# Optimization experiments

Hardware: AMD Instinct MI355X
Metric: run time of the kernel (lower is better)

Reference implementation:

```python
import jax, jax.numpy as jnp
import numpy as np

H = 1024  # n_hidden
T = 8192  # sequence length


def setup_inputs() -> dict:
    key = jax.random.key(0)
    ks = jax.random.split(key, 11)
    s = 1.0 / np.sqrt(H)  # torch LSTMCell/Linear default init scale
    u = lambda k, shape: jax.random.uniform(k, shape, jnp.float32, -s, s)
    return {
        "sequence": jax.random.normal(ks[0], (1, T), jnp.float32),
        # lstm1: input size 1 -> hidden H
        "w_ih1": u(ks[1], (4 * H, 1)),
        "w_hh1": u(ks[2], (4 * H, H)),
        "b_ih1": u(ks[3], (4 * H,)),
        "b_hh1": u(ks[4], (4 * H,)),
        # lstm2: hidden H -> hidden H
        "w_ih2": u(ks[5], (4 * H, H)),
        "w_hh2": u(ks[6], (4 * H, H)),
        "b_ih2": u(ks[7], (4 * H,)),
        "b_hh2": u(ks[8], (4 * H,)),
        # final linear: H -> 1
        "w_lin": u(ks[9], (1, H)),
        "b_lin": u(ks[10], (1,)),
    }


def _lstm_cell(x, h, c, w_ih, w_hh, b_ih, b_hh):
    # x: [1, in], h/c: [1, H]. PyTorch LSTMCell gate order: i, f, g, o
    gates = x @ w_ih.T + h @ w_hh.T + (b_ih + b_hh)  # [1, 4H]
    i, f, g, o = jnp.split(gates, 4, axis=-1)
    i = jax.nn.sigmoid(i)
    f = jax.nn.sigmoid(f)
    g = jnp.tanh(g)
    o = jax.nn.sigmoid(o)
    c_new = f * c + i * g
    h_new = o * jnp.tanh(c_new)
    return h_new, c_new


def reference(sequence, w_ih1, w_hh1, b_ih1, b_hh1,
              w_ih2, w_hh2, b_ih2, b_hh2, w_lin, b_lin):
    n = sequence.shape[0]  # 1
    z = jnp.zeros((n, w_hh1.shape[1]), jnp.float32)
    init = (z, z, z, z)  # h1, c1, h2, c2
    xs = sequence.T[:, :, None]  # [T, 1, 1] timesteps

    def step(carry, x_t):
        h1, c1, h2, c2 = carry
        h1, c1 = _lstm_cell(x_t, h1, c1, w_ih1, w_hh1, b_ih1, b_hh1)
        h2, c2 = _lstm_cell(h1, h2, c2, w_ih2, w_hh2, b_ih2, b_hh2)
        out = h2 @ w_lin.T + b_lin  # [1, 1]
        return (h1, c1, h2, c2), out

    _, outputs = jax.lax.scan(step, init, xs)
    return outputs  # [T, 1, 1] — stacked version of the original list of [1,1] outputs
```

## Files before the change

kernel.cpp:

```cpp
#include <hip/hip_runtime.h>

#define HID   1024
#define SEQT  8192
#define NBLK  256
#define TPB   512

#define WS_BYTES 32768

typedef float v16f __attribute__((ext_vector_type(16)));
typedef unsigned long long u64;

__device__ __forceinline__ float sig_(float x) { return 1.0f / (1.0f + expf(-x)); }

__device__ __forceinline__ u64 ldp(const u64* p) {
    return __hip_atomic_load(p, __ATOMIC_RELAXED, __HIP_MEMORY_SCOPE_AGENT);
}
__device__ __forceinline__ void stp(u64* p, u64 v) {
    __hip_atomic_store(p, v, __ATOMIC_RELAXED, __HIP_MEMORY_SCOPE_AGENT);
}

extern "C" __global__ void __launch_bounds__(TPB, 2)
lstm_hyb(const float* __restrict__ seq,
         const float* __restrict__ w_ih1, const float* __restrict__ w_hh1,
         const float* __restrict__ b_ih1, const float* __restrict__ b_hh1,
         const float* __restrict__ w_ih2, const float* __restrict__ w_hh2,
         const float* __restrict__ b_ih2, const float* __restrict__ b_hh2,
         const float* __restrict__ w_lin, const float* __restrict__ b_lin,
         float* __restrict__ out, u64* ws)
{
    __shared__ float h1s[HID];
    __shared__ float h2s[HID];
    __shared__ float seqs[SEQT];

    const int  lane = threadIdx.x & 63;
    const int  widx = threadIdx.x >> 6;
    const bool isL1 = (widx < 4);
    const int  r    = blockIdx.x * 4 + (widx & 3);

    u64* h1t = ws;
    u64* h2t = ws + 2048;

    for (int i = threadIdx.x; i < SEQT; i += TPB) seqs[i] = seq[i];

    const float* bA  = isL1 ? w_hh1 : w_ih2;
    const float* bB  = isL1 ? w_hh1 : w_hh2;
    const float* bbi = isL1 ? b_ih1 : b_ih2;
    const float* bbh = isL1 ? b_hh1 : b_hh2;
    const float  zmask = isL1 ? 0.f : 1.f;
    const float  xsel  = isL1 ? 1.f : 0.f;

    v16f A0, A1, A2, A3, B0, B1, B2, B3;
    {
        const size_t ro = (size_t)r * HID + lane;
        const float *a0 = bA + ro, *a1 = bA + (size_t)HID * HID + ro,
                    *a2 = bA + 2 * (size_t)HID * HID + ro, *a3 = bA + 3 * (size_t)HID * HID + ro;
        const float *b0 = bB + ro, *b1 = bB + (size_t)HID * HID + ro,
                    *b2 = bB + 2 * (size_t)HID * HID + ro, *b3 = bB + 3 * (size_t)HID * HID + ro;
#pragma unroll
        for (int k = 0; k < 16; ++k) {
            A0[k] = a0[64 * k]; A1[k] = a1[64 * k]; A2[k] = a2[64 * k]; A3[k] = a3[64 * k];
            B0[k] = b0[64 * k]; B1[k] = b1[64 * k]; B2[k] = b2[64 * k]; B3[k] = b3[64 * k];
        }
    }
    const float wx0 = w_ih1[0 * HID + r], wx1 = w_ih1[1 * HID + r],
                wx2 = w_ih1[2 * HID + r], wx3 = w_ih1[3 * HID + r];
    const float bb0 = bbi[0 * HID + r] + bbh[0 * HID + r];
    const float bb1 = bbi[1 * HID + r] + bbh[1 * HID + r];
    const float bb2 = bbi[2 * HID + r] + bbh[2 * HID + r];
    const float bb3 = bbi[3 * HID + r] + bbh[3 * HID + r];

    const bool carrier = (blockIdx.x == 0 && widx == 7);
    v16f WL; float blin = 0.f;
#pragma unroll
    for (int k = 0; k < 16; ++k) WL[k] = 0.f;
    if (carrier) {
#pragma unroll
        for (int k = 0; k < 16; ++k) WL[k] = w_lin[lane + 64 * k];
        blin = b_lin[0];
    }

    u64* pub = isL1 ? h1t : h2t;
    float c = 0.f;

    for (int t = 0; t <= SEQT + 1; ++t) {
        if (widx == 0 && t <= SEQT) {
            const u64* p = h1t + ((t + 1) & 1) * HID + lane;
            int guard = 0;
            for (;;) {
                int mn = 0x7fffffff;
#pragma unroll
                for (int k = 0; k < 16; ++k) {
                    u64 q = ldp(p + 64 * k);
                    h1s[lane + 64 * k] = __uint_as_float((unsigned)q);
                    mn = min(mn, (int)(q >> 32));
                }
                if (__all(mn >= t)) break;
                if (++guard > (1 << 14)) break;
            }
        }
        if (widx == 4) {
            const u64* p = h2t + (t & 1) * HID + lane;
            const int thr = t - 1;
            int guard = 0;
            for (;;) {
                int mn = 0x7fffffff;
#pragma unroll
                for (int k = 0; k < 16; ++k) {
                    u64 q = ldp(p + 64 * k);
                    h2s[lane + 64 * k] = __uint_as_float((unsigned)q);
                    mn = min(mn, (int)(q >> 32));
                }
                if (__all(mn >= thr)) break;
                if (++guard > (1 << 14)) break;
            }
        }
        __syncthreads();

        const bool act = isL1 ? (t < SEQT) : (t >= 1 && t <= SEQT);
        if (act) {
            v16f v1, v2;
#pragma unroll
            for (int k = 0; k < 16; ++k) {
                v1[k] = h1s[lane + 64 * k];
                v2[k] = h2s[lane + 64 * k] * zmask;
            }
            float a0 = 0.f, a1 = 0.f, a2 = 0.f, a3 = 0.f;
#pragma unroll
            for (int k = 0; k < 16; ++k) {
                a0 = fmaf(A0[k], v1[k], a0);
                a1 = fmaf(A1[k], v1[k], a1);
                a2 = fmaf(A2[k], v1[k], a2);
                a3 = fmaf(A3[k], v1[k], a3);
            }
#pragma unroll
            for (int k = 0; k < 16; ++k) {
                a0 = fmaf(B0[k], v2[k], a0);
                a1 = fmaf(B1[k], v2[k], a1);
                a2 = fmaf(B2[k], v2[k], a2);
                a3 = fmaf(B3[k], v2[k], a3);
            }
#pragma unroll
            for (int s = 32; s; s >>= 1) {
                a0 += __shfl_xor(a0, s);
                a1 += __shfl_xor(a1, s);
                a2 += __shfl_xor(a2, s);
                a3 += __shfl_xor(a3, s);
            }
            const float xg = xsel * ((t < SEQT) ? seqs[t] : 0.f);
            float i_ = sig_(a0 + xg * wx0 + bb0);
            float f_ = sig_(a1 + xg * wx1 + bb1);
            float g_ = tanhf(a2 + xg * wx2 + bb2);
            float o_ = sig_(a3 + xg * wx3 + bb3);
            c = f_ * c + i_ * g_;
            float h = o_ * tanhf(c);
            if (lane == 0) {
                const int ps = isL1 ? t : (t - 1);
                stp(pub + (ps & 1) * HID + r,
                    ((u64)(unsigned)(ps + 1) << 32) | (u64)__float_as_uint(h));
            }
        }

        if (carrier && t >= 2) {
            float ov = 0.f;
#pragma unroll
            for (int k = 0; k < 16; ++k) ov = fmaf(WL[k], h2s[lane + 64 * k], ov);
#pragma unroll
            for (int s = 32; s; s >>= 1) ov += __shfl_xor(ov, s);
            if (lane == 0) out[t - 2] = ov + blin;
        }

        __syncthreads();
    }
}

extern "C" void kernel_launch(void* const* d_in, const int* in_sizes, int n_in,
                              void* d_out, int out_size, void* d_ws, size_t ws_size,
                              hipStream_t stream)
{
    (void)hipMemsetAsync(d_ws, 0, WS_BYTES, stream);

    const float* seq  = (const float*)d_in[0];
    const float* wih1 = (const float*)d_in[1];
    const float* whh1 = (const float*)d_in[2];
    const float* bih1 = (const float*)d_in[3];
    const float* bhh1 = (const float*)d_in[4];
    const float* wih2 = (const float*)d_in[5];
    const float* whh2 = (const float*)d_in[6];
    const float* bih2 = (const float*)d_in[7];
    const float* bhh2 = (const float*)d_in[8];
    const float* wlin = (const float*)d_in[9];
    const float* blin = (const float*)d_in[10];
    float* out = (float*)d_out;
    u64*   ws  = (u64*)d_ws;

    hipLaunchKernelGGL(lstm_hyb, dim3(NBLK), dim3(TPB), 0, stream,
                       seq, wih1, whh1, bih1, bhh1,
                       wih2, whh2, bih2, bhh2, wlin, blin,
                       out, ws);
}
```

Measured before the change: 25.42 ms.

## Split polling across all warps and double-buffer LDS to drop second barrier

Each of the four layer-1 warps and four layer-2 warps now polls one quarter of the published hidden-state vector, where before a single warp per layer fetched all 1024 entries. The shared-memory h1/h2 buffers are double-buffered by timestep parity, which lets the trailing __syncthreads per step be removed. Together these shorten the serial fetch latency and cut one block barrier per timestep on the critical path. The spin guard is halved, and the double buffering relies on the leading barrier alone to order reads against next-step writes.

```diff
diff --git a/kernel.cpp b/kernel.cpp
--- a/kernel.cpp
+++ b/kernel.cpp
@@ -20,22 +20,23 @@
 }
 
 extern "C" __global__ void __launch_bounds__(TPB, 2)
-lstm_hyb(const float* __restrict__ seq,
-         const float* __restrict__ w_ih1, const float* __restrict__ w_hh1,
-         const float* __restrict__ b_ih1, const float* __restrict__ b_hh1,
-         const float* __restrict__ w_ih2, const float* __restrict__ w_hh2,
-         const float* __restrict__ b_ih2, const float* __restrict__ b_hh2,
-         const float* __restrict__ w_lin, const float* __restrict__ b_lin,
-         float* __restrict__ out, u64* ws)
+lstm_split(const float* __restrict__ seq,
+           const float* __restrict__ w_ih1, const float* __restrict__ w_hh1,
+           const float* __restrict__ b_ih1, const float* __restrict__ b_hh1,
+           const float* __restrict__ w_ih2, const float* __restrict__ w_hh2,
+           const float* __restrict__ b_ih2, const float* __restrict__ b_hh2,
+           const float* __restrict__ w_lin, const float* __restrict__ b_lin,
+           float* __restrict__ out, u64* ws)
 {
-    __shared__ float h1s[HID];
-    __shared__ float h2s[HID];
+    __shared__ float h1s[2][HID];
+    __shared__ float h2s[2][HID];
     __shared__ float seqs[SEQT];
 
     const int  lane = threadIdx.x & 63;
     const int  widx = threadIdx.x >> 6;
+    const int  blk  = blockIdx.x;
     const bool isL1 = (widx < 4);
-    const int  r    = blockIdx.x * 4 + (widx & 3);
+    const int  r    = blk * 4 + (widx & 3);
 
     u64* h1t = ws;
     u64* h2t = ws + 2048;
@@ -69,7 +70,7 @@
     const float bb2 = bbi[2 * HID + r] + bbh[2 * HID + r];
     const float bb3 = bbi[3 * HID + r] + bbh[3 * HID + r];
 
-    const bool carrier = (blockIdx.x == 0 && widx == 7);
+    const bool carrier = (blk == 0 && widx == 7);
     v16f WL; float blin = 0.f;
 #pragma unroll
     for (int k = 0; k < 16; ++k) WL[k] = 0.f;
@@ -83,35 +84,44 @@
     float c = 0.f;
 
     for (int t = 0; t <= SEQT + 1; ++t) {
-        if (widx == 0 && t <= SEQT) {
-            const u64* p = h1t + ((t + 1) & 1) * HID + lane;
-            int guard = 0;
-            for (;;) {
-                int mn = 0x7fffffff;
-#pragma unroll
-                for (int k = 0; k < 16; ++k) {
-                    u64 q = ldp(p + 64 * k);
-                    h1s[lane + 64 * k] = __uint_as_float((unsigned)q);
-                    mn = min(mn, (int)(q >> 32));
+        const int cur = t & 1;
+
+        if (isL1) {
+            if (t <= SEQT) {
+                const int base = widx * 256 + lane;
+                const u64* p = h1t + ((t + 1) & 1) * HID + base;
+                float* dst = &h1s[cur][base];
+                int guard = 0;
+                for (;;) {
+                    u64 q0 = ldp(p);       u64 q1 = ldp(p + 64);
+                    u64 q2 = ldp(p + 128); u64 q3 = ldp(p + 192);
+                    dst[0]   = __uint_as_float((unsigned)q0);
+                    dst[64]  = __uint_as_float((unsigned)q1);
+                    dst[128] = __uint_as_float((unsigned)q2);
+                    dst[192] = __uint_as_float((unsigned)q3);
+                    int mn = min(min((int)(q0 >> 32), (int)(q1 >> 32)),
+                                 min((int)(q2 >> 32), (int)(q3 >> 32)));
+                    if (__all(mn >= t)) break;
+                    if (++guard > (1 << 13)) break;
                 }
-                if (__all(mn >= t)) break;
-                if (++guard > (1 << 14)) break;
-            }
-        }
-        if (widx == 4) {
-            const u64* p = h2t + (t & 1) * HID + lane;
+            }
+        } else {
+            const int base = (widx - 4) * 256 + lane;
+            const u64* p = h2t + cur * HID + base;
+            float* dst = &h2s[cur][base];
             const int thr = t - 1;
             int guard = 0;
             for (;;) {
-                int mn = 0x7fffffff;
-#pragma unroll
-                for (int k = 0; k < 16; ++k) {
-                    u64 q = ldp(p + 64 * k);
-                    h2s[lane + 64 * k] = __uint_as_float((unsigned)q);
-                    mn = min(mn, (int)(q >> 32));
-                }
+                u64 q0 = ldp(p);       u64 q1 = ldp(p + 64);
+                u64 q2 = ldp(p + 128); u64 q3 = ldp(p + 192);
+                dst[0]   = __uint_as_float((unsigned)q0);
+                dst[64]  = __uint_as_float((unsigned)q1);
+                dst[128] = __uint_as_float((unsigned)q2);
+                dst[192] = __uint_as_float((unsigned)q3);
+                int mn = min(min((int)(q0 >> 32), (int)(q1 >> 32)),
+                             min((int)(q2 >> 32), (int)(q3 >> 32)));
                 if (__all(mn >= thr)) break;
-                if (++guard > (1 << 14)) break;
+                if (++guard > (1 << 13)) break;
             }
         }
         __syncthreads();
@@ -121,8 +131,8 @@
             v16f v1, v2;
 #pragma unroll
             for (int k = 0; k < 16; ++k) {
-                v1[k] = h1s[lane + 64 * k];
-                v2[k] = h2s[lane + 64 * k] * zmask;
+                v1[k] = h1s[cur][lane + 64 * k];
+                v2[k] = h2s[cur][lane + 64 * k] * zmask;
             }
             float a0 = 0.f, a1 = 0.f, a2 = 0.f, a3 = 0.f;
 #pragma unroll
@@ -163,13 +173,11 @@
         if (carrier && t >= 2) {
             float ov = 0.f;
 #pragma unroll
-            for (int k = 0; k < 16; ++k) ov = fmaf(WL[k], h2s[lane + 64 * k], ov);
+            for (int k = 0; k < 16; ++k) ov = fmaf(WL[k], h2s[cur][lane + 64 * k], ov);
 #pragma unroll
             for (int s = 32; s; s >>= 1) ov += __shfl_xor(ov, s);
             if (lane == 0) out[t - 2] = ov + blin;
         }
-
-        __syncthreads();
     }
 }
 
@@ -193,7 +201,7 @@
     float* out = (float*)d_out;
     u64*   ws  = (u64*)d_ws;
 
-    hipLaunchKernelGGL(lstm_hyb, dim3(NBLK), dim3(TPB), 0, stream,
+    hipLaunchKernelGGL(lstm_split, dim3(NBLK), dim3(TPB), 0, stream,
                        seq, wih1, whh1, bih1, bhh1,
                        wih2, whh2, bih2, bhh2, wlin, blin,
                        out, ws);
```

After: 46.84 ms. 1.84x slower.

## Store LSTM gate weights as fp16 in shared memory instead of registers

Applied to the files above, without the earlier changes.

Each wave's gate-weight slice is converted to fp16 once at startup and stored interleaved in LDS as 8-wide vectors. Each step reads it back and accumulates in fp32, replacing the 128 fp32 weight registers per thread. The aim is to relieve register pressure, since the launch bounds cap VGPRs and the old layout likely spilled. The polling loops also issue all sixteen atomic loads before writing to shared memory, so their latencies overlap. The costs are fp16 rounding of the weights across a long recurrence, extra LDS reads on the per-step critical path, and roughly 136KB of LDS per block, which allows only one block per CU.

```diff
diff --git a/kernel.cpp b/kernel.cpp
--- a/kernel.cpp
+++ b/kernel.cpp
@@ -8,6 +8,7 @@
 #define WS_BYTES 32768
 
 typedef float v16f __attribute__((ext_vector_type(16)));
+typedef _Float16 f16x8 __attribute__((ext_vector_type(8)));
 typedef unsigned long long u64;
 
 __device__ __forceinline__ float sig_(float x) { return 1.0f / (1.0f + expf(-x)); }
@@ -20,7 +21,7 @@
 }
 
 extern "C" __global__ void __launch_bounds__(TPB, 2)
-lstm_hyb(const float* __restrict__ seq,
+lstm_w16(const float* __restrict__ seq,
          const float* __restrict__ w_ih1, const float* __restrict__ w_hh1,
          const float* __restrict__ b_ih1, const float* __restrict__ b_hh1,
          const float* __restrict__ w_ih2, const float* __restrict__ w_hh2,
@@ -28,40 +29,59 @@
          const float* __restrict__ w_lin, const float* __restrict__ b_lin,
          float* __restrict__ out, u64* ws)
 {
+    __shared__ f16x8 wA[8][8][64];
+    __shared__ f16x8 wB[4][8][64];
     __shared__ float h1s[HID];
     __shared__ float h2s[HID];
     __shared__ float seqs[SEQT];
 
     const int  lane = threadIdx.x & 63;
     const int  widx = threadIdx.x >> 6;
+    const int  blk  = blockIdx.x;
     const bool isL1 = (widx < 4);
-    const int  r    = blockIdx.x * 4 + (widx & 3);
+    const int  r    = blk * 4 + (widx & 3);
 
     u64* h1t = ws;
     u64* h2t = ws + 2048;
 
     for (int i = threadIdx.x; i < SEQT; i += TPB) seqs[i] = seq[i];
 
-    const float* bA  = isL1 ? w_hh1 : w_ih2;
-    const float* bB  = isL1 ? w_hh1 : w_hh2;
+    if (isL1) {
+#pragma unroll
+        for (int j = 0; j < 8; ++j) {
+            f16x8 w;
+#pragma unroll
+            for (int g = 0; g < 4; ++g) {
+                const float* row = w_hh1 + (size_t)(g * HID + r) * HID;
+                w[2 * g]     = (_Float16)row[lane + 128 * j];
+                w[2 * g + 1] = (_Float16)row[lane + 128 * j + 64];
+            }
+            wA[widx][j][lane] = w;
+        }
+    } else {
+#pragma unroll
+        for (int j = 0; j < 8; ++j) {
+            f16x8 wi, wh;
+#pragma unroll
+            for (int g = 0; g < 4; ++g) {
+                const float* ri = w_ih2 + (size_t)(g * HID + r) * HID;
+                const float* rh = w_hh2 + (size_t)(g * HID + r) * HID;
+                wi[2 * g]     = (_Float16)ri[lane + 128 * j];
+                wi[2 * g + 1] = (_Float16)ri[lane + 128 * j + 64];
+                wh[2 * g]     = (_Float16)rh[lane + 128 * j];
+                wh[2 * g + 1] = (_Float16)rh[lane + 128 * j + 64];
+            }
+            wA[widx][j][lane]     = wi;
+            wB[widx - 4][j][lane] = wh;
+        }
+    }
+    const f16x8* wAp = &wA[widx][0][0];
+    const f16x8* wBp = isL1 ? wAp : &wB[widx - 4][0][0];
+    const float  zmask = isL1 ? 0.f : 1.f;
+    const float  xsel  = isL1 ? 1.f : 0.f;
+
     const float* bbi = isL1 ? b_ih1 : b_ih2;
     const float* bbh = isL1 ? b_hh1 : b_hh2;
-    const float  zmask = isL1 ? 0.f : 1.f;
-    const float  xsel  = isL1 ? 1.f : 0.f;
-
-    v16f A0, A1, A2, A3, B0, B1, B2, B3;
-    {
-        const size_t ro = (size_t)r * HID + lane;
-        const float *a0 = bA + ro, *a1 = bA + (size_t)HID * HID + ro,
-                    *a2 = bA + 2 * (size_t)HID * HID + ro, *a3 = bA + 3 * (size_t)HID * HID + ro;
-        const float *b0 = bB + ro, *b1 = bB + (size_t)HID * HID + ro,
-                    *b2 = bB + 2 * (size_t)HID * HID + ro, *b3 = bB + 3 * (size_t)HID * HID + ro;
-#pragma unroll
-        for (int k = 0; k < 16; ++k) {
-            A0[k] = a0[64 * k]; A1[k] = a1[64 * k]; A2[k] = a2[64 * k]; A3[k] = a3[64 * k];
-            B0[k] = b0[64 * k]; B1[k] = b1[64 * k]; B2[k] = b2[64 * k]; B3[k] = b3[64 * k];
-        }
-    }
     const float wx0 = w_ih1[0 * HID + r], wx1 = w_ih1[1 * HID + r],
                 wx2 = w_ih1[2 * HID + r], wx3 = w_ih1[3 * HID + r];
     const float bb0 = bbi[0 * HID + r] + bbh[0 * HID + r];
@@ -69,7 +89,7 @@
     const float bb2 = bbi[2 * HID + r] + bbh[2 * HID + r];
     const float bb3 = bbi[3 * HID + r] + bbh[3 * HID + r];
 
-    const bool carrier = (blockIdx.x == 0 && widx == 7);
+    const bool carrier = (blk == 0 && widx == 7);
     v16f WL; float blin = 0.f;
 #pragma unroll
     for (int k = 0; k < 16; ++k) WL[k] = 0.f;
@@ -88,12 +108,15 @@
             int guard = 0;
             for (;;) {
                 int mn = 0x7fffffff;
+                u64 q[16];
 #pragma unroll
                 for (int k = 0; k < 16; ++k) {
-                    u64 q = ldp(p + 64 * k);
-                    h1s[lane + 64 * k] = __uint_as_float((unsigned)q);
-                    mn = min(mn, (int)(q >> 32));
+                    q[k] = ldp(p + 64 * k);
+                    mn = min(mn, (int)(q[k] >> 32));
                 }
+#pragma unroll
+                for (int k = 0; k < 16; ++k)
+                    h1s[lane + 64 * k] = __uint_as_float((unsigned)q[k]);
                 if (__all(mn >= t)) break;
                 if (++guard > (1 << 14)) break;
             }
@@ -104,12 +127,15 @@
             int guard = 0;
             for (;;) {
                 int mn = 0x7fffffff;
+                u64 q[16];
 #pragma unroll
                 for (int k = 0; k < 16; ++k) {
-                    u64 q = ldp(p + 64 * k);
-                    h2s[lane + 64 * k] = __uint_as_float((unsigned)q);
-                    mn = min(mn, (int)(q >> 32));
+                    q[k] = ldp(p + 64 * k);
+                    mn = min(mn, (int)(q[k] >> 32));
                 }
+#pragma unroll
+                for (int k = 0; k < 16; ++k)
+                    h2s[lane + 64 * k] = __uint_as_float((unsigned)q[k]);
                 if (__all(mn >= thr)) break;
                 if (++guard > (1 << 14)) break;
             }
@@ -126,18 +152,28 @@
             }
             float a0 = 0.f, a1 = 0.f, a2 = 0.f, a3 = 0.f;
 #pragma unroll
-            for (int k = 0; k < 16; ++k) {
-                a0 = fmaf(A0[k], v1[k], a0);
-                a1 = fmaf(A1[k], v1[k], a1);
-                a2 = fmaf(A2[k], v1[k], a2);
-                a3 = fmaf(A3[k], v1[k], a3);
-            }
-#pragma unroll
-            for (int k = 0; k < 16; ++k) {
-                a0 = fmaf(B0[k], v2[k], a0);
-                a1 = fmaf(B1[k], v2[k], a1);
-                a2 = fmaf(B2[k], v2[k], a2);
-                a3 = fmaf(B3[k], v2[k], a3);
+            for (int j = 0; j < 8; ++j) {
+                const f16x8 w = wAp[j * 64 + lane];
+                a0 = fmaf((float)w[0], v1[2 * j],     a0);
+                a0 = fmaf((float)w[1], v1[2 * j + 1], a0);
+                a1 = fmaf((float)w[2], v1[2 * j],     a1);
+                a1 = fmaf((float)w[3], v1[2 * j + 1], a1);
+                a2 = fmaf((float)w[4], v1[2 * j],     a2);
+                a2 = fmaf((float)w[5], v1[2 * j + 1], a2);
+                a3 = fmaf((float)w[6], v1[2 * j],     a3);
+                a3 = fmaf((float)w[7], v1[2 * j + 1], a3);
+            }
+#pragma unroll
+            for (int j = 0; j < 8; ++j) {
+                const f16x8 w = wBp[j * 64 + lane];
+                a0 = fmaf((float)w[0], v2[2 * j],     a0);
+                a0 = fmaf((float)w[1], v2[2 * j + 1], a0);
+                a1 = fmaf((float)w[2], v2[2 * j],     a1);
+                a1 = fmaf((float)w[3], v2[2 * j + 1], a1);
+                a2 = fmaf((float)w[4], v2[2 * j],     a2);
+                a2 = fmaf((float)w[5], v2[2 * j + 1], a2);
+                a3 = fmaf((float)w[6], v2[2 * j],     a3);
+                a3 = fmaf((float)w[7], v2[2 * j + 1], a3);
             }
 #pragma unroll
             for (int s = 32; s; s >>= 1) {
@@ -193,7 +229,7 @@
     float* out = (float*)d_out;
     u64*   ws  = (u64*)d_ws;
 
-    hipLaunchKernelGGL(lstm_hyb, dim3(NBLK), dim3(TPB), 0, stream,
+    hipLaunchKernelGGL(lstm_w16, dim3(NBLK), dim3(TPB), 0, stream,
                        seq, wih1, whh1, bih1, bhh1,
                        wih2, whh2, bih2, bhh2, wlin, blin,
                        out, ws);
```

New measurement: 29.66 ms. +16.7%, slower.
